# Kernel tuning notes

Measured on AMD Instinct MI355X. Metric: run time of the kernel, lower is better.

Reference implementation:

```python
import jax, jax.numpy as jnp
import numpy as np

NUM_CELLS = 2048
CELL_DIM = 256
N_STATES = 131072


def setup_inputs() -> dict:
    key = jax.random.key(0)
    k1, k2 = jax.random.split(key)
    x = jax.random.normal(k1, (N_STATES, CELL_DIM), dtype=jnp.float32)
    placeCells = jax.random.normal(k2, (NUM_CELLS, CELL_DIM), dtype=jnp.float32)
    return {"x": x, "placeCells": placeCells}


def reference(x, placeCells):
    # states: (N, cellDim); sims: (N, numCells); output: (N,) int argmax
    states = x.reshape(-1, CELL_DIM)
    sims = jnp.matmul(states, placeCells.T)  # (N, numCells) dense similarity
    return jnp.argmax(sims, axis=1)
```

## Files before the change

kernel.cpp:

```cpp
#include <hip/hip_runtime.h>
#include <float.h>
#include <stdint.h>

#define NUM_CELLS 2048
#define CELL_DIM  256
#define N_STATES  131072

typedef _Float16 half8 __attribute__((ext_vector_type(8)));
typedef float    f32x4 __attribute__((ext_vector_type(4)));
typedef float    f32x4v __attribute__((ext_vector_type(4)));

#define M1 0.10f
#define M2 0.0008f
#define CAP1 32768
#define CAP2 4096

#define WS_C1 0
#define WS_C2 4
#define WS_L1 1024
#define WS_L2 (WS_L1 + 4 * CAP1)
#define WS_PH 262144
#define WS_PL (WS_PH + 1048576)
#define WS_NEEDED (WS_PL + 1048576 + 131072)

__global__ void prep_p(const float* __restrict__ p, _Float16* __restrict__ ph,
                       _Float16* __restrict__ pl, int* __restrict__ c1,
                       int* __restrict__ c2) {
    int d = blockIdx.x * 256 + threadIdx.x;
    if (d == 0) { *c1 = 0; *c2 = 0; }
    int l = d & 63, kf = (d >> 6) & 7, ct = d >> 9;
    int cell = ct * 16 + (l & 15);
    int k0 = kf * 32 + (l >> 4) * 8;
    const float* s = p + cell * 256 + k0;
    float4 a = *(const float4*)s, b = *(const float4*)(s + 4);
    float v[8] = {a.x, a.y, a.z, a.w, b.x, b.y, b.z, b.w};
    half8 h, lo;
#pragma unroll
    for (int j = 0; j < 8; ++j) {
        _Float16 hi = (_Float16)v[j];
        h[j] = hi;
        lo[j] = (_Float16)((v[j] - (float)hi) * 2048.0f);
    }
    *(half8*)(ph + (size_t)d * 8) = h;
    *(half8*)(pl + (size_t)d * 8) = lo;
}

__launch_bounds__(512, 2)
__global__ void pc_gemm1(const float* __restrict__ x, const _Float16* __restrict__ ph,
                         int* __restrict__ out, int* __restrict__ c1,
                         int* __restrict__ l1) {
    __shared__ _Float16 smem[32768];

    const int tid = threadIdx.x;
    const int l = tid & 63;
    const int w = tid >> 6;
    const int wr = w >> 2, wc = w & 3;

    const float* xg = x + (size_t)blockIdx.x * (128 * CELL_DIM);
#pragma unroll
    for (int i = 0; i < 8; ++i) {
        int d = tid + i * 512;
        int dl = d & 63, kf = (d >> 6) & 7, rt = d >> 9;
        int row = rt * 16 + (dl & 15);
        int k0 = kf * 32 + (dl >> 4) * 8;
        const f32x4v* s = (const f32x4v*)(xg + row * 256 + k0);
        f32x4v a = __builtin_nontemporal_load(s);
        f32x4v b = __builtin_nontemporal_load(s + 1);
        half8 h;
        h[0] = (_Float16)a[0]; h[1] = (_Float16)a[1];
        h[2] = (_Float16)a[2]; h[3] = (_Float16)a[3];
        h[4] = (_Float16)b[0]; h[5] = (_Float16)b[1];
        h[6] = (_Float16)b[2]; h[7] = (_Float16)b[3];
        *(half8*)(smem + d * 8) = h;
    }
    __syncthreads();

    half8 A[4][8];
#pragma unroll
    for (int rt = 0; rt < 4; ++rt)
#pragma unroll
        for (int kf = 0; kf < 8; ++kf)
            A[rt][kf] = *(const half8*)(smem + (((wr * 4 + rt) * 8 + kf) * 64 + l) * 8);
    __syncthreads();

    const _Float16* bb = ph + wc * 4096 + (size_t)l * 8;

    half8 Bf[8];
#pragma unroll
    for (int j = 0; j < 8; ++j) Bf[j] = *(const half8*)(bb + j * 512);

    float t1[16], t2[16];
    int ic[16];
#pragma unroll
    for (int s = 0; s < 16; ++s) { t1[s] = -FLT_MAX; t2[s] = -FLT_MAX; ic[s] = 0; }

    for (int t = 0; t < 32; ++t) {
        const _Float16* bn = bb + (t + 1) * 16384;
        f32x4 a0 = {}, a1 = {}, a2 = {}, a3 = {};
#pragma unroll
        for (int k = 0; k < 8; ++k) {
            half8 B = Bf[k];
            Bf[k] = *(const half8*)(bn + k * 512);
            a0 = __builtin_amdgcn_mfma_f32_16x16x32_f16(A[0][k], B, a0, 0, 0, 0);
            a1 = __builtin_amdgcn_mfma_f32_16x16x32_f16(A[1][k], B, a1, 0, 0, 0);
            a2 = __builtin_amdgcn_mfma_f32_16x16x32_f16(A[2][k], B, a2, 0, 0, 0);
            a3 = __builtin_amdgcn_mfma_f32_16x16x32_f16(A[3][k], B, a3, 0, 0, 0);
        }
#define UPD(ACC, RT)                                                       \
        _Pragma("unroll")                                                  \
        for (int reg = 0; reg < 4; ++reg) {                                \
            int s = (RT) * 4 + reg;                                        \
            float v = (ACC)[reg];                                          \
            float nt2 = __builtin_amdgcn_fmed3f(t1[s], t2[s], v);          \
            ic[s] = (v > t1[s]) ? t : ic[s];                               \
            t1[s] = fmaxf(t1[s], v);                                       \
            t2[s] = nt2;                                                   \
        }
        UPD(a0, 0) UPD(a1, 1) UPD(a2, 2) UPD(a3, 3)
#undef UPD
    }

    int idx[16];
#pragma unroll
    for (int s = 0; s < 16; ++s) idx[s] = (ic[s] * 4 + wc) * 16 + (l & 15);
#pragma unroll
    for (int m = 1; m <= 8; m <<= 1) {
#pragma unroll
        for (int s = 0; s < 16; ++s) {
            float ot1 = __shfl_xor(t1[s], m, 64);
            int   oi  = __shfl_xor(idx[s], m, 64);
            float ot2 = __shfl_xor(t2[s], m, 64);
            float nt2 = fmaxf(fminf(t1[s], ot1), fmaxf(t2[s], ot2));
            if (ot1 > t1[s] || (ot1 == t1[s] && oi < idx[s])) { t1[s] = ot1; idx[s] = oi; }
            t2[s] = nt2;
        }
    }

    float* rT1 = (float*)smem;
    int*   rI1 = (int*)smem + 512;
    float* rT2 = (float*)smem + 1024;
    if ((l & 15) == 0) {
#pragma unroll
        for (int rt = 0; rt < 4; ++rt)
#pragma unroll
            for (int reg = 0; reg < 4; ++reg) {
                int s = rt * 4 + reg;
                int row = wr * 64 + rt * 16 + (l >> 4) * 4 + reg;
                rT1[row * 4 + wc] = t1[s];
                rI1[row * 4 + wc] = idx[s];
                rT2[row * 4 + wc] = t2[s];
            }
    }
    __syncthreads();
    if (tid < 128) {
        float T1 = -FLT_MAX, T2 = -FLT_MAX; int I1 = 0x7FFFFFFF;
#pragma unroll
        for (int g = 0; g < 4; ++g) {
            float v1 = rT1[tid * 4 + g];
            int   vi = rI1[tid * 4 + g];
            float v2 = rT2[tid * 4 + g];
            float nt2 = fmaxf(fminf(T1, v1), fmaxf(T2, v2));
            if (v1 > T1 || (v1 == T1 && vi < I1)) { T1 = v1; I1 = vi; }
            T2 = nt2;
        }
        int grow = blockIdx.x * 128 + tid;
        out[grow] = I1;
        bool f = (T1 - T2 < M1);
        unsigned long long msk = __ballot(f);
        int cnt = __popcll(msk);
        int prefix = __popcll(msk & ((1ull << l) - 1ull));
        int bpos = 0;
        if (l == 0 && cnt) bpos = atomicAdd(c1, cnt);
        bpos = __shfl(bpos, 0, 64);
        if (f) {
            int pos = bpos + prefix;
            if (pos < CAP1) l1[pos] = grow;
        }
    }
}

__launch_bounds__(256, 2)
__global__ void pc_rescue2(const float* __restrict__ x, const _Float16* __restrict__ ph,
                           const _Float16* __restrict__ pl,
                           const int* __restrict__ c1, const int* __restrict__ l1,
                           int* __restrict__ out, int* __restrict__ c2,
                           int* __restrict__ l2) {
    const int n0 = *c1;
    const int n = n0 < CAP1 ? n0 : CAP1;
    const int G = (n + 15) >> 4;
    const int tid = threadIdx.x;
    const int l = tid & 63, wc = tid >> 6;

    __shared__ float rT1[64];
    __shared__ int   rI1[64];
    __shared__ float rT2[64];

    for (int g = blockIdx.x; g < G; g += gridDim.x) {
        const int base = g * 16;
        __syncthreads();

        const int rslot = base + (l & 15);
        const int my_row = l1[rslot < n ? rslot : (n - 1)];

        half8 Ah[8], Al[8];
#pragma unroll
        for (int kf = 0; kf < 8; ++kf) {
            const float* s = x + (size_t)my_row * 256 + kf * 32 + (l >> 4) * 8;
            float4 a = *(const float4*)s, b = *(const float4*)(s + 4);
            float v[8] = {a.x, a.y, a.z, a.w, b.x, b.y, b.z, b.w};
#pragma unroll
            for (int j = 0; j < 8; ++j) {
                _Float16 hi = (_Float16)v[j];
                Ah[kf][j] = hi;
                Al[kf][j] = (_Float16)((v[j] - (float)hi) * 2048.0f);
            }
        }

        const _Float16* bh = ph + wc * 4096 + (size_t)l * 8;
        const _Float16* bl = pl + wc * 4096 + (size_t)l * 8;
        half8 BH[4], BL[4];
#pragma unroll
        for (int j = 0; j < 4; ++j) {
            BH[j] = *(const half8*)(bh + j * 512);
            BL[j] = *(const half8*)(bl + j * 512);
        }

        float t1[4], t2[4];
        int ic[4];
#pragma unroll
        for (int s = 0; s < 4; ++s) { t1[s] = -FLT_MAX; t2[s] = -FLT_MAX; ic[s] = 0; }

        for (int t = 0; t < 32; ++t) {
            const _Float16* bth = bh + t * 16384;
            const _Float16* btl = bl + t * 16384;
            f32x4 hh = {}, hl = {}, lh = {};
#pragma unroll
            for (int k = 0; k < 8; ++k) {
                half8 Bh_ = BH[k & 3], Bl_ = BL[k & 3];
                int off = (k < 4) ? (k + 4) * 512 : (16384 + (k - 4) * 512);
                BH[k & 3] = *(const half8*)(bth + off);
                BL[k & 3] = *(const half8*)(btl + off);
                hh = __builtin_amdgcn_mfma_f32_16x16x32_f16(Ah[k], Bh_, hh, 0, 0, 0);
                hl = __builtin_amdgcn_mfma_f32_16x16x32_f16(Ah[k], Bl_, hl, 0, 0, 0);
                lh = __builtin_amdgcn_mfma_f32_16x16x32_f16(Al[k], Bh_, lh, 0, 0, 0);
            }
#pragma unroll
            for (int reg = 0; reg < 4; ++reg) {
                float v = hh[reg] + (hl[reg] + lh[reg]) * (1.0f / 2048.0f);
                float nt2 = __builtin_amdgcn_fmed3f(t1[reg], t2[reg], v);
                ic[reg] = (v > t1[reg]) ? t : ic[reg];
                t1[reg] = fmaxf(t1[reg], v);
                t2[reg] = nt2;
            }
        }

        int idx[4];
#pragma unroll
        for (int s = 0; s < 4; ++s) idx[s] = (ic[s] * 4 + wc) * 16 + (l & 15);
#pragma unroll
        for (int m = 1; m <= 8; m <<= 1) {
#pragma unroll
            for (int s = 0; s < 4; ++s) {
                float ot1 = __shfl_xor(t1[s], m, 64);
                int   oi  = __shfl_xor(idx[s], m, 64);
                float ot2 = __shfl_xor(t2[s], m, 64);
                float nt2 = fmaxf(fminf(t1[s], ot1), fmaxf(t2[s], ot2));
                if (ot1 > t1[s] || (ot1 == t1[s] && oi < idx[s])) { t1[s] = ot1; idx[s] = oi; }
                t2[s] = nt2;
            }
        }

        if ((l & 15) == 0) {
#pragma unroll
            for (int reg = 0; reg < 4; ++reg) {
                int r = (l >> 4) * 4 + reg;
                rT1[r * 4 + wc] = t1[reg];
                rI1[r * 4 + wc] = idx[reg];
                rT2[r * 4 + wc] = t2[reg];
            }
        }
        __syncthreads();
        if (tid < 16) {
            float T1 = -FLT_MAX, T2 = -FLT_MAX; int I1 = 0x7FFFFFFF;
#pragma unroll
            for (int q = 0; q < 4; ++q) {
                float v1 = rT1[tid * 4 + q];
                int   vi = rI1[tid * 4 + q];
                float v2 = rT2[tid * 4 + q];
                float nt2 = fmaxf(fminf(T1, v1), fmaxf(T2, v2));
                if (v1 > T1 || (v1 == T1 && vi < I1)) { T1 = v1; I1 = vi; }
                T2 = nt2;
            }
            int slot = base + tid;
            if (slot < n) {
                int grow = l1[slot];
                out[grow] = I1;
                if (T1 - T2 < M2) {
                    int pos = atomicAdd(c2, 1);
                    if (pos < CAP2) l2[pos] = grow;
                }
            }
        }
    }
}

__global__ void rescue3(const float* __restrict__ x, const float* __restrict__ p,
                        const int* __restrict__ count, const int* __restrict__ list,
                        int* __restrict__ out) {
    __shared__ float xrow[256];
    __shared__ float pch[32][260];
    __shared__ float red2[32][9];
    __shared__ float bvs[32];
    __shared__ int   bis[32];
    const int tid = threadIdx.x;
    const int n0 = *count;
    const int n = n0 < CAP2 ? n0 : CAP2;
    for (int e = blockIdx.x; e < n; e += gridDim.x) {
        const int row = list[e];
        __syncthreads();
        if (tid < 64) {
            float4 v = *(const float4*)(x + (size_t)row * 256 + tid * 4);
            *(float4*)(&xrow[tid * 4]) = v;
        }
        float bv = -FLT_MAX; int bi = 0;
        const int cell = tid & 31, kq = tid >> 5;
        for (int c0 = 0; c0 < NUM_CELLS; c0 += 32) {
            __syncthreads();
#pragma unroll
            for (int i = 0; i < 8; ++i) {
                int f = tid + i * 256;
                int cr = f >> 6, k4 = (f & 63) * 4;
                float4 v = *(const float4*)(p + (size_t)(c0 + cr) * 256 + k4);
                *(float4*)(&pch[cr][k4]) = v;
            }
            __syncthreads();
            float s = 0.f;
#pragma unroll
            for (int j = 0; j < 8; ++j) {
                float4 pv = *(const float4*)(&pch[cell][kq * 32 + j * 4]);
                float4 xv = *(const float4*)(&xrow[kq * 32 + j * 4]);
                s = fmaf(xv.x, pv.x, s); s = fmaf(xv.y, pv.y, s);
                s = fmaf(xv.z, pv.z, s); s = fmaf(xv.w, pv.w, s);
            }
            red2[cell][kq] = s;
            __syncthreads();
            if (tid < 32) {
                float dot = 0.f;
#pragma unroll
                for (int q = 0; q < 8; ++q) dot += red2[tid][q];
                if (dot > bv) { bv = dot; bi = c0 + tid; }
            }
        }
        if (tid < 32) { bvs[tid] = bv; bis[tid] = bi; }
        __syncthreads();
        if (tid == 0) {
            float B = bvs[0]; int BI = bis[0];
#pragma unroll
            for (int t = 1; t < 32; ++t)
                if (bvs[t] > B || (bvs[t] == B && bis[t] < BI)) { B = bvs[t]; BI = bis[t]; }
            out[row] = BI;
        }
    }
}

#define BM 64
#define BN 64
#define BK 32
#define XP 260
#define PP 68
__launch_bounds__(256, 2)
__global__ void placecells_argmax_fp32(const float* __restrict__ x,
                                       const float* __restrict__ pc,
                                       int* __restrict__ out) {
    __shared__ float xs[BM * XP];
    __shared__ float ps[BK * PP];
    const int tid = threadIdx.x;
    const int tx = tid & 15;
    const int ty = tid >> 4;
    const float* xg = x + (size_t)blockIdx.x * (BM * CELL_DIM);
#pragma unroll
    for (int i = 0; i < 16; ++i) {
        int f = tid + i * 256;
        int s = f >> 6, k4 = (f & 63) << 2;
        *(float4*)(&xs[s * XP + k4]) = *(const float4*)(xg + s * CELL_DIM + k4);
    }
    __syncthreads();
    float runv[4]; int runi[4];
#pragma unroll
    for (int si = 0; si < 4; ++si) { runv[si] = -FLT_MAX; runi[si] = 0; }
    for (int jc = 0; jc < NUM_CELLS; jc += BN) {
        float acc[4][4];
#pragma unroll
        for (int si = 0; si < 4; ++si)
#pragma unroll
            for (int cj = 0; cj < 4; ++cj) acc[si][cj] = 0.0f;
        for (int kc = 0; kc < CELL_DIM; kc += BK) {
            __syncthreads();
#pragma unroll
            for (int i = 0; i < 2; ++i) {
                int f = tid + i * 256;
                int c = f >> 3, k4 = (f & 7) << 2;
                float4 v = *(const float4*)(pc + (size_t)(jc + c) * CELL_DIM + kc + k4);
                ps[(k4 + 0) * PP + c] = v.x; ps[(k4 + 1) * PP + c] = v.y;
                ps[(k4 + 2) * PP + c] = v.z; ps[(k4 + 3) * PP + c] = v.w;
            }
            __syncthreads();
#pragma unroll
            for (int kk = 0; kk < BK; kk += 4) {
                float4 xv[4];
#pragma unroll
                for (int si = 0; si < 4; ++si)
                    xv[si] = *(const float4*)(&xs[(ty * 4 + si) * XP + kc + kk]);
#pragma unroll
                for (int kt = 0; kt < 4; ++kt) {
                    float4 pv = *(const float4*)(&ps[(kk + kt) * PP + tx * 4]);
#pragma unroll
                    for (int si = 0; si < 4; ++si) {
                        float xk = (kt == 0) ? xv[si].x : (kt == 1) ? xv[si].y :
                                   (kt == 2) ? xv[si].z : xv[si].w;
                        acc[si][0] = fmaf(xk, pv.x, acc[si][0]);
                        acc[si][1] = fmaf(xk, pv.y, acc[si][1]);
                        acc[si][2] = fmaf(xk, pv.z, acc[si][2]);
                        acc[si][3] = fmaf(xk, pv.w, acc[si][3]);
                    }
                }
            }
        }
#pragma unroll
        for (int si = 0; si < 4; ++si)
#pragma unroll
            for (int cj = 0; cj < 4; ++cj) {
                int idx = jc + tx * 4 + cj;
                if (acc[si][cj] > runv[si]) { runv[si] = acc[si][cj]; runi[si] = idx; }
            }
    }
    __syncthreads();
    float* rv = ps; int* ri = (int*)(ps + 1024);
#pragma unroll
    for (int si = 0; si < 4; ++si) {
        int s = ty * 4 + si;
        rv[s * 16 + tx] = runv[si]; ri[s * 16 + tx] = runi[si];
    }
    __syncthreads();
    if (tid < BM) {
        float bv = rv[tid * 16]; int bi = ri[tid * 16];
#pragma unroll
        for (int t = 1; t < 16; ++t) {
            float v = rv[tid * 16 + t]; int i = ri[tid * 16 + t];
            if (v > bv || (v == bv && i < bi)) { bv = v; bi = i; }
        }
        out[(size_t)blockIdx.x * BM + tid] = bi;
    }
}

extern "C" void kernel_launch(void* const* d_in, const int* in_sizes, int n_in,
                              void* d_out, int out_size, void* d_ws, size_t ws_size,
                              hipStream_t stream) {
    const float* x  = (const float*)d_in[0];
    const float* pc = (const float*)d_in[1];
    int* out = (int*)d_out;

    if (ws_size >= (size_t)WS_NEEDED) {
        char* ws = (char*)d_ws;
        int* c1 = (int*)(ws + WS_C1);
        int* c2 = (int*)(ws + WS_C2);
        int* l1 = (int*)(ws + WS_L1);
        int* l2 = (int*)(ws + WS_L2);
        _Float16* ph = (_Float16*)(ws + WS_PH);
        _Float16* pl = (_Float16*)(ws + WS_PL);
        prep_p<<<256, 256, 0, stream>>>(pc, ph, pl, c1, c2);
        pc_gemm1<<<N_STATES / 128, 512, 0, stream>>>(x, ph, out, c1, l1);
        pc_rescue2<<<256, 256, 0, stream>>>(x, ph, pl, c1, l1, out, c2, l2);
        rescue3<<<64, 256, 0, stream>>>(x, pc, c2, l2, out);
    } else {
        placecells_argmax_fp32<<<N_STATES / BM, 256, 0, stream>>>(x, pc, out);
    }
}
```

Baseline: 499.2 us.

## Stage place-cell B tiles into LDS via async global_load_lds double buffering

```diff
diff --git a/kernel.cpp b/kernel.cpp
--- a/kernel.cpp
+++ b/kernel.cpp
@@ -22,6 +22,9 @@
 #define WS_PH 262144
 #define WS_PL (WS_PH + 1048576)
 #define WS_NEEDED (WS_PL + 1048576 + 131072)
+
+#define AS1 __attribute__((address_space(1)))
+#define AS3 __attribute__((address_space(3)))
 
 __global__ void prep_p(const float* __restrict__ p, _Float16* __restrict__ ph,
                        _Float16* __restrict__ pl, int* __restrict__ c1,
@@ -83,24 +86,46 @@
             A[rt][kf] = *(const half8*)(smem + (((wr * 4 + rt) * 8 + kf) * 64 + l) * 8);
     __syncthreads();
 
-    const _Float16* bb = ph + wc * 4096 + (size_t)l * 8;
-
-    half8 Bf[8];
-#pragma unroll
-    for (int j = 0; j < 8; ++j) Bf[j] = *(const half8*)(bb + j * 512);
+    const char* phb = (const char*)ph;
+    char* lds = (char*)smem;
+
+    {
+        const char* src = phb + w * 1024 + (size_t)l * 16;
+        char* dst = lds + w * 1024;
+#pragma unroll
+        for (int i = 0; i < 4; ++i)
+            __builtin_amdgcn_global_load_lds((const AS1 void*)(src + i * 8192),
+                                             (AS3 void*)(dst + i * 8192), 16, 0, 0);
+    }
+    __syncthreads();
 
     float t1[16], t2[16];
     int ic[16];
 #pragma unroll
     for (int s = 0; s < 16; ++s) { t1[s] = -FLT_MAX; t2[s] = -FLT_MAX; ic[s] = 0; }
 
+    int cur = 0;
     for (int t = 0; t < 32; ++t) {
-        const _Float16* bn = bb + (t + 1) * 16384;
+        {
+            int tn = (t + 1) & 31;
+            const char* src = phb + (size_t)tn * 32768 + w * 1024 + (size_t)l * 16;
+            char* dst = lds + (cur ^ 1) * 32768 + w * 1024;
+#pragma unroll
+            for (int i = 0; i < 4; ++i)
+                __builtin_amdgcn_global_load_lds((const AS1 void*)(src + i * 8192),
+                                                 (AS3 void*)(dst + i * 8192), 16, 0, 0);
+        }
+
+        const char* bp = lds + cur * 32768 + wc * 8192 + l * 16;
+        half8 Bf[8];
+#pragma unroll
+        for (int k = 0; k < 8; ++k)
+            Bf[k] = *(const half8*)(bp + k * 1024);
+
         f32x4 a0 = {}, a1 = {}, a2 = {}, a3 = {};
 #pragma unroll
         for (int k = 0; k < 8; ++k) {
             half8 B = Bf[k];
-            Bf[k] = *(const half8*)(bn + k * 512);
             a0 = __builtin_amdgcn_mfma_f32_16x16x32_f16(A[0][k], B, a0, 0, 0, 0);
             a1 = __builtin_amdgcn_mfma_f32_16x16x32_f16(A[1][k], B, a1, 0, 0, 0);
             a2 = __builtin_amdgcn_mfma_f32_16x16x32_f16(A[2][k], B, a2, 0, 0, 0);
@@ -118,6 +143,9 @@
         }
         UPD(a0, 0) UPD(a1, 1) UPD(a2, 2) UPD(a3, 3)
 #undef UPD
+
+        __syncthreads();
+        cur ^= 1;
     }
 
     int idx[16];
```

After: 479.8 us. 3.9% less time.

## Stage placeCells tiles through an LDS ring with async global-to-LDS loads

Applied to the files above, without the earlier changes.

```diff
diff --git a/kernel.cpp b/kernel.cpp
--- a/kernel.cpp
+++ b/kernel.cpp
@@ -22,6 +22,9 @@
 #define WS_PH 262144
 #define WS_PL (WS_PH + 1048576)
 #define WS_NEEDED (WS_PL + 1048576 + 131072)
+
+#define AS1 __attribute__((address_space(1)))
+#define AS3 __attribute__((address_space(3)))
 
 __global__ void prep_p(const float* __restrict__ p, _Float16* __restrict__ ph,
                        _Float16* __restrict__ pl, int* __restrict__ c1,
@@ -45,88 +48,116 @@
     *(half8*)(pl + (size_t)d * 8) = lo;
 }
 
-__launch_bounds__(512, 2)
+__launch_bounds__(256, 2)
 __global__ void pc_gemm1(const float* __restrict__ x, const _Float16* __restrict__ ph,
                          int* __restrict__ out, int* __restrict__ c1,
                          int* __restrict__ l1) {
-    __shared__ _Float16 smem[32768];
+    __shared__ _Float16 ringmem[32768];
+    char* ring = (char*)ringmem;
 
     const int tid = threadIdx.x;
     const int l = tid & 63;
     const int w = tid >> 6;
-    const int wr = w >> 2, wc = w & 3;
-
-    const float* xg = x + (size_t)blockIdx.x * (128 * CELL_DIM);
-#pragma unroll
-    for (int i = 0; i < 8; ++i) {
-        int d = tid + i * 512;
-        int dl = d & 63, kf = (d >> 6) & 7, rt = d >> 9;
-        int row = rt * 16 + (dl & 15);
-        int k0 = kf * 32 + (dl >> 4) * 8;
-        const f32x4v* s = (const f32x4v*)(xg + row * 256 + k0);
-        f32x4v a = __builtin_nontemporal_load(s);
-        f32x4v b = __builtin_nontemporal_load(s + 1);
-        half8 h;
-        h[0] = (_Float16)a[0]; h[1] = (_Float16)a[1];
-        h[2] = (_Float16)a[2]; h[3] = (_Float16)a[3];
-        h[4] = (_Float16)b[0]; h[5] = (_Float16)b[1];
-        h[6] = (_Float16)b[2]; h[7] = (_Float16)b[3];
-        *(half8*)(smem + d * 8) = h;
-    }
-    __syncthreads();
-
-    half8 A[4][8];
-#pragma unroll
-    for (int rt = 0; rt < 4; ++rt)
-#pragma unroll
-        for (int kf = 0; kf < 8; ++kf)
-            A[rt][kf] = *(const half8*)(smem + (((wr * 4 + rt) * 8 + kf) * 64 + l) * 8);
-    __syncthreads();
-
-    const _Float16* bb = ph + wc * 4096 + (size_t)l * 8;
-
-    half8 Bf[8];
-#pragma unroll
-    for (int j = 0; j < 8; ++j) Bf[j] = *(const half8*)(bb + j * 512);
-
-    float t1[16], t2[16];
-    int ic[16];
-#pragma unroll
-    for (int s = 0; s < 16; ++s) { t1[s] = -FLT_MAX; t2[s] = -FLT_MAX; ic[s] = 0; }
-
-    for (int t = 0; t < 32; ++t) {
-        const _Float16* bn = bb + (t + 1) * 16384;
-        f32x4 a0 = {}, a1 = {}, a2 = {}, a3 = {};
+
+    const char* phb = (const char*)ph;
+
+#pragma unroll
+    for (int ss = 0; ss < 3; ++ss) {
+        const char* src = phb + ss * 16384 + w * 4096 + (size_t)l * 16;
+        char* dst = ring + ss * 16384 + w * 4096;
+#pragma unroll
+        for (int i = 0; i < 4; ++i)
+            __builtin_amdgcn_global_load_lds((const AS1 void*)(src + i * 1024),
+                                             (AS3 void*)(dst + i * 1024), 16, 0, 0);
+    }
+    asm volatile("s_waitcnt vmcnt(4)" ::: "memory");
+
+    const int wrow = blockIdx.x * 128 + w * 32;
+    half8 A[2][8];
+#pragma unroll
+    for (int rt = 0; rt < 2; ++rt)
+#pragma unroll
+        for (int kf = 0; kf < 8; ++kf) {
+            const f32x4v* sp = (const f32x4v*)(x +
+                (size_t)(wrow + rt * 16 + (l & 15)) * 256 + kf * 32 + (l >> 4) * 8);
+            f32x4v a = __builtin_nontemporal_load(sp);
+            f32x4v b = __builtin_nontemporal_load(sp + 1);
+            half8 h;
+            h[0] = (_Float16)a[0]; h[1] = (_Float16)a[1];
+            h[2] = (_Float16)a[2]; h[3] = (_Float16)a[3];
+            h[4] = (_Float16)b[0]; h[5] = (_Float16)b[1];
+            h[6] = (_Float16)b[2]; h[7] = (_Float16)b[3];
+            A[rt][kf] = h;
+        }
+
+    asm volatile("s_barrier" ::: "memory");
+
+    const int lofs = l * 16;
+    half8 Bf0[8], Bf1[8];
+#pragma unroll
+    for (int k = 0; k < 8; ++k) {
+        Bf0[k] = *(const half8*)(ring + k * 1024 + lofs);
+        Bf1[k] = *(const half8*)(ring + 8192 + k * 1024 + lofs);
+    }
+
+    float t1[8], t2[8];
+    int ic[8];
+#pragma unroll
+    for (int s = 0; s < 8; ++s) { t1[s] = -FLT_MAX; t2[s] = -FLT_MAX; ic[s] = 0; }
+
+    for (int t = 0; t < 64; ++t) {
+        {
+            int tn = (t + 3) & 63;
+            const char* src = phb + (size_t)tn * 16384 + w * 4096 + (size_t)l * 16;
+            char* dst = ring + ((t + 3) & 3) * 16384 + w * 4096;
+#pragma unroll
+            for (int i = 0; i < 4; ++i)
+                __builtin_amdgcn_global_load_lds((const AS1 void*)(src + i * 1024),
+                                                 (AS3 void*)(dst + i * 1024), 16, 0, 0);
+        }
+
+        const char* nbp = ring + ((t + 1) & 3) * 16384 + lofs;
+
+        f32x4 a00 = {}, a10 = {}, a01 = {}, a11 = {};
 #pragma unroll
         for (int k = 0; k < 8; ++k) {
-            half8 B = Bf[k];
-            Bf[k] = *(const half8*)(bn + k * 512);
-            a0 = __builtin_amdgcn_mfma_f32_16x16x32_f16(A[0][k], B, a0, 0, 0, 0);
-            a1 = __builtin_amdgcn_mfma_f32_16x16x32_f16(A[1][k], B, a1, 0, 0, 0);
-            a2 = __builtin_amdgcn_mfma_f32_16x16x32_f16(A[2][k], B, a2, 0, 0, 0);
-            a3 = __builtin_amdgcn_mfma_f32_16x16x32_f16(A[3][k], B, a3, 0, 0, 0);
-        }
-#define UPD(ACC, RT)                                                       \
-        _Pragma("unroll")                                                  \
-        for (int reg = 0; reg < 4; ++reg) {                                \
-            int s = (RT) * 4 + reg;                                        \
-            float v = (ACC)[reg];                                          \
-            float nt2 = __builtin_amdgcn_fmed3f(t1[s], t2[s], v);          \
-            ic[s] = (v > t1[s]) ? t : ic[s];                               \
-            t1[s] = fmaxf(t1[s], v);                                       \
-            t2[s] = nt2;                                                   \
-        }
-        UPD(a0, 0) UPD(a1, 1) UPD(a2, 2) UPD(a3, 3)
-#undef UPD
-    }
-
-    int idx[16];
-#pragma unroll
-    for (int s = 0; s < 16; ++s) idx[s] = (ic[s] * 4 + wc) * 16 + (l & 15);
+            a00 = __builtin_amdgcn_mfma_f32_16x16x32_f16(A[0][k], Bf0[k], a00, 0, 0, 0);
+            a10 = __builtin_amdgcn_mfma_f32_16x16x32_f16(A[1][k], Bf0[k], a10, 0, 0, 0);
+            Bf0[k] = *(const half8*)(nbp + k * 1024);
+            a01 = __builtin_amdgcn_mfma_f32_16x16x32_f16(A[0][k], Bf1[k], a01, 0, 0, 0);
+            a11 = __builtin_amdgcn_mfma_f32_16x16x32_f16(A[1][k], Bf1[k], a11, 0, 0, 0);
+            Bf1[k] = *(const half8*)(nbp + 8192 + k * 1024);
+        }
+
+#define UPD2(V, TR, CODE)                                                  \
+        {                                                                  \
+            float v = (V);                                                 \
+            float nt2 = __builtin_amdgcn_fmed3f(t1[TR], t2[TR], v);        \
+            ic[TR] = (v > t1[TR]) ? (CODE) : ic[TR];                       \
+            t1[TR] = fmaxf(t1[TR], v);                                     \
+            t2[TR] = nt2;                                                  \
+        }
+#pragma unroll
+        for (int reg = 0; reg < 4; ++reg) {
+            UPD2(a00[reg], reg,     t * 2)
+            UPD2(a01[reg], reg,     t * 2 + 1)
+            UPD2(a10[reg], 4 + reg, t * 2)
+            UPD2(a11[reg], 4 + reg, t * 2 + 1)
+        }
+#undef UPD2
+
+        asm volatile("s_waitcnt vmcnt(4)\n\ts_barrier" ::: "memory");
+    }
+
+    asm volatile("s_waitcnt vmcnt(0)" ::: "memory");
+
+    int idx[8];
+#pragma unroll
+    for (int s = 0; s < 8; ++s) idx[s] = ic[s] * 16 + (l & 15);
 #pragma unroll
     for (int m = 1; m <= 8; m <<= 1) {
 #pragma unroll
-        for (int s = 0; s < 16; ++s) {
+        for (int s = 0; s < 8; ++s) {
             float ot1 = __shfl_xor(t1[s], m, 64);
             int   oi  = __shfl_xor(idx[s], m, 64);
             float ot2 = __shfl_xor(t2[s], m, 64);
@@ -136,45 +167,24 @@
         }
     }
 
-    float* rT1 = (float*)smem;
-    int*   rI1 = (int*)smem + 512;
-    float* rT2 = (float*)smem + 1024;
-    if ((l & 15) == 0) {
-#pragma unroll
-        for (int rt = 0; rt < 4; ++rt)
-#pragma unroll
-            for (int reg = 0; reg < 4; ++reg) {
-                int s = rt * 4 + reg;
-                int row = wr * 64 + rt * 16 + (l >> 4) * 4 + reg;
-                rT1[row * 4 + wc] = t1[s];
-                rI1[row * 4 + wc] = idx[s];
-                rT2[row * 4 + wc] = t2[s];
-            }
-    }
-    __syncthreads();
-    if (tid < 128) {
-        float T1 = -FLT_MAX, T2 = -FLT_MAX; int I1 = 0x7FFFFFFF;
-#pragma unroll
-        for (int g = 0; g < 4; ++g) {
-            float v1 = rT1[tid * 4 + g];
-            int   vi = rI1[tid * 4 + g];
-            float v2 = rT2[tid * 4 + g];
-            float nt2 = fmaxf(fminf(T1, v1), fmaxf(T2, v2));
-            if (v1 > T1 || (v1 == T1 && vi < I1)) { T1 = v1; I1 = vi; }
-            T2 = nt2;
-        }
-        int grow = blockIdx.x * 128 + tid;
-        out[grow] = I1;
-        bool f = (T1 - T2 < M1);
+#pragma unroll
+    for (int s = 0; s < 8; ++s) {
+        int rt = s >> 2, reg = s & 3;
+        int row = wrow + rt * 16 + (l >> 4) * 4 + reg;
+        bool vld = (l & 15) == 0;
+        if (vld) out[row] = idx[s];
+        bool f = vld && (t1[s] - t2[s] < M1);
         unsigned long long msk = __ballot(f);
         int cnt = __popcll(msk);
-        int prefix = __popcll(msk & ((1ull << l) - 1ull));
-        int bpos = 0;
-        if (l == 0 && cnt) bpos = atomicAdd(c1, cnt);
-        bpos = __shfl(bpos, 0, 64);
-        if (f) {
-            int pos = bpos + prefix;
-            if (pos < CAP1) l1[pos] = grow;
+        if (cnt) {
+            int prefix = __popcll(msk & ((1ull << l) - 1ull));
+            int bpos = 0;
+            if (l == 0) bpos = atomicAdd(c1, cnt);
+            bpos = __shfl(bpos, 0, 64);
+            if (f) {
+                int pos = bpos + prefix;
+                if (pos < CAP1) l1[pos] = row;
+            }
         }
     }
 }
@@ -469,7 +479,7 @@
         _Float16* ph = (_Float16*)(ws + WS_PH);
         _Float16* pl = (_Float16*)(ws + WS_PL);
         prep_p<<<256, 256, 0, stream>>>(pc, ph, pl, c1, c2);
-        pc_gemm1<<<N_STATES / 128, 512, 0, stream>>>(x, ph, out, c1, l1);
+        pc_gemm1<<<N_STATES / 128, 256, 0, stream>>>(x, ph, out, c1, l1);
         pc_rescue2<<<256, 256, 0, stream>>>(x, ph, pl, c1, l1, out, c2, l2);
         rescue3<<<64, 256, 0, stream>>>(x, pc, c2, l2, out);
     } else {
```

Result: faster. 444.2 us (-11.0%).
